# Kernel optimization log

Hardware: AMD Instinct MI355X
Metric: run time of the kernel (lower is better)

Reference implementation:

```python
import jax, jax.numpy as jnp
import numpy as np

FRACTION = 0.33  # from attn_type='query_selector_0.33'


def setup_inputs() -> dict:
    key = jax.random.key(0)
    k1, k2, k3, k4 = jax.random.split(key, 4)
    B, L, DIM_VAL, DIM_ATTN = 8, 4096, 64, 64
    scale = 1.0 / np.sqrt(DIM_VAL).astype(np.float32)
    x = jax.random.normal(k1, (B, L, DIM_VAL), dtype=jnp.float32)
    Wq = jax.random.normal(k2, (DIM_VAL, DIM_ATTN), dtype=jnp.float32) * scale
    Wk = jax.random.normal(k3, (DIM_VAL, DIM_ATTN), dtype=jnp.float32) * scale
    Wv = jax.random.normal(k4, (DIM_VAL, DIM_VAL), dtype=jnp.float32) * scale
    return {"x": x, "Wq": Wq, "Wk": Wk, "Wv": Wv}


def reference(x, Wq, Wk, Wv):
    # Projections (bias-free Linears)
    Q = jnp.einsum('bld,de->ble', x, Wq)  # [B, L, Da]
    K = jnp.einsum('bld,de->ble', x, Wk)  # [B, L, Da]
    V = jnp.einsum('bld,de->ble', x, Wv)  # [B, L, Dv]

    B, L_Q, Da = Q.shape
    l_Q = int((1.0 - FRACTION) * L_Q)  # static: shapes known at trace time

    # keys.topk(l_Q, dim=1).values -> per-channel top-l_Q along seq; mean over them
    K_top = jax.lax.top_k(jnp.swapaxes(K, 1, 2), l_Q)[0]  # [B, Da, l_Q]
    K_reduce = K_top.mean(axis=-1)                         # [B, Da]

    # score each query against the reduced key; pick top-l_Q queries
    sqk = jnp.einsum('bd,bld->bl', K_reduce, Q)            # [B, L_Q]
    indices = jax.lax.top_k(sqk, l_Q)[1]                   # [B, l_Q] int32

    # gather sampled queries
    Q_sample = jnp.take_along_axis(Q, indices[:, :, None], axis=1)  # [B, l_Q, Da]

    # dense attention for the sampled queries only
    scores = jnp.einsum('bqd,bkd->bqk', Q_sample, K) / jnp.sqrt(jnp.asarray(Da, Q.dtype))
    attn = jax.nn.softmax(scores, axis=-1)                 # [B, l_Q, L]
    out_sel = jnp.einsum('bqk,bkv->bqv', attn, V)          # [B, l_Q, Dv]

    # mean-filled result, scatter attention outputs to selected rows
    mean_values = V.mean(axis=-2)                          # [B, Dv]
    result = jnp.broadcast_to(mean_values[:, None, :], (B, L_Q, V.shape[-1]))
    result = result.at[jnp.arange(B)[:, None], indices].set(out_sel)
    return result
```

## Files before the change

kernel.cpp:

```cpp
#include <hip/hip_runtime.h>
#include <hip/hip_bf16.h>
#include <math.h>

#define BATCH 8
#define SEQ   4096
#define DIM   64
#define LQ    2744
#define QPB   128
#define NQB   22
#define QPAD  2816
#define KS    8
#define L2E   1.4426950408889634f
#define QSC   0.1803368801111204f

typedef _Float16 half8 __attribute__((ext_vector_type(8)));
typedef short    bs8   __attribute__((ext_vector_type(8)));
typedef float    fx16  __attribute__((ext_vector_type(16)));
typedef unsigned short ushort_t;

union UH { uint4 u4; half8 h; };
union UB { unsigned u[4]; uint4 u4; bs8 s; };

__device__ __forceinline__ unsigned pack_bf16(float a, float b) {
    unsigned ua = __float_as_uint(a), ub = __float_as_uint(b);
    ua += 0x7FFFu + ((ua >> 16) & 1u);
    ub += 0x7FFFu + ((ub >> 16) & 1u);
    return (ua >> 16) | (ub & 0xFFFF0000u);
}

__device__ __forceinline__ unsigned f2sort(float f) {
    unsigned u = __float_as_uint(f);
    return (u & 0x80000000u) ? ~u : (u | 0x80000000u);
}
__device__ __forceinline__ float sort2f(unsigned u) {
    return __uint_as_float((u & 0x80000000u) ? (u & 0x7FFFFFFFu) : ~u);
}

template <int NT>
__device__ void radix_select_4096(const unsigned* u, int k, unsigned* hist,
                                  unsigned* scan, unsigned* res) {
    const int t = threadIdx.x;
    if (t == 0) { res[0] = 0u; res[1] = (unsigned)k; }
    for (int pass = 3; pass >= 0; --pass) {
        const int shift = pass * 8;
        if (t < 256) hist[t] = 0u;
        __syncthreads();
        const unsigned pref  = res[0];
        const unsigned kk    = res[1];
        const unsigned hmask = (pass == 3) ? 0u : (0xFFFFFFFFu << (shift + 8));
        for (int i = t; i < 4096; i += NT) {
            unsigned ui = u[i];
            if ((ui & hmask) == pref) atomicAdd(&hist[(ui >> shift) & 255u], 1u);
        }
        __syncthreads();
        unsigned h = 0u, s = 0u;
        if (t < 256) { h = hist[t]; s = h; scan[t] = s; }
        __syncthreads();
#pragma unroll
        for (int ofs = 1; ofs < 256; ofs <<= 1) {
            unsigned add = (t < 256 && t + ofs < 256) ? scan[t + ofs] : 0u;
            __syncthreads();
            if (t < 256) { s += add; scan[t] = s; }
            __syncthreads();
        }
        if (t < 256 && s >= kk && (s - h) < kk) {
            res[0] = pref | ((unsigned)t << shift);
            res[1] = kk - (s - h);
        }
        __syncthreads();
    }
}

__global__ __launch_bounds__(256) void proj_kernel(
    const float* __restrict__ x,  const float* __restrict__ Wq,
    const float* __restrict__ Wk, const float* __restrict__ Wv,
    float* __restrict__ Q, float* __restrict__ Kt,
    _Float16* __restrict__ Qh, _Float16* __restrict__ Kh,
    ushort_t* __restrict__ Vt, float* __restrict__ pmean) {
    const int rt = blockIdx.x, b = blockIdx.y, t = threadIdx.x;
    __shared__ float4 xs4[64 * 17];
    __shared__ float  red[4][64];
    {
        const float4* xg = (const float4*)(x + ((size_t)b * SEQ + rt * 64) * DIM);
        for (int i = 0; i < 4; ++i) {
            int s = t + 256 * i;
            xs4[(s >> 4) * 17 + (s & 15)] = xg[s];
        }
    }
    __syncthreads();
    const int ch = t & 63, rg = t >> 6;
    float accq[16], acck[16], accv[16];
#pragma unroll
    for (int i = 0; i < 16; ++i) { accq[i] = 0.f; acck[i] = 0.f; accv[i] = 0.f; }
    for (int dc = 0; dc < 4; ++dc) {
        float wq[16], wk[16], wv[16];
#pragma unroll
        for (int dd = 0; dd < 16; ++dd) {
            int d = dc * 16 + dd;
            wq[dd] = Wq[d * 64 + ch]; wk[dd] = Wk[d * 64 + ch]; wv[dd] = Wv[d * 64 + ch];
        }
        for (int r = 0; r < 16; ++r) {
            const int row = rg * 16 + r;
            const float4* xr = &xs4[row * 17 + dc * 4];
            float xv[16];
            float4 a0 = xr[0], a1 = xr[1], a2 = xr[2], a3 = xr[3];
            xv[0]=a0.x; xv[1]=a0.y; xv[2]=a0.z; xv[3]=a0.w;
            xv[4]=a1.x; xv[5]=a1.y; xv[6]=a1.z; xv[7]=a1.w;
            xv[8]=a2.x; xv[9]=a2.y; xv[10]=a2.z; xv[11]=a2.w;
            xv[12]=a3.x; xv[13]=a3.y; xv[14]=a3.z; xv[15]=a3.w;
#pragma unroll
            for (int dd = 0; dd < 16; ++dd) {
                accq[r] = fmaf(xv[dd], wq[dd], accq[r]);
                acck[r] = fmaf(xv[dd], wk[dd], acck[r]);
                accv[r] = fmaf(xv[dd], wv[dd], accv[r]);
            }
        }
    }
    const int rowbase = rt * 64 + rg * 16;
    float sv = 0.f;
#pragma unroll
    for (int r = 0; r < 16; ++r) {
        size_t o = ((size_t)b * SEQ + rowbase + r) * DIM + ch;
        Q[o]  = accq[r];
        Qh[o] = (_Float16)(accq[r] * QSC);
        Kh[o] = (_Float16)acck[r];
        sv += accv[r];
    }
    float4* ktp = (float4*)(Kt + ((size_t)b * 64 + ch) * SEQ + rowbase);
    ktp[0] = make_float4(acck[0], acck[1], acck[2], acck[3]);
    ktp[1] = make_float4(acck[4], acck[5], acck[6], acck[7]);
    ktp[2] = make_float4(acck[8], acck[9], acck[10], acck[11]);
    ktp[3] = make_float4(acck[12], acck[13], acck[14], acck[15]);
    {
        unsigned pk[8];
#pragma unroll
        for (int i = 0; i < 8; ++i) {
            __hip_bfloat162 h2 = __float22bfloat162_rn(make_float2(accv[2*i], accv[2*i+1]));
            union { __hip_bfloat162 h; unsigned u; } cv; cv.h = h2;
            pk[i] = cv.u;
        }
        uint4* vp = (uint4*)(Vt + ((size_t)(b * 64 + ch)) * SEQ + rowbase);
        vp[0] = make_uint4(pk[0], pk[1], pk[4], pk[5]);
        vp[1] = make_uint4(pk[2], pk[3], pk[6], pk[7]);
    }
    red[rg][ch] = sv;
    __syncthreads();
    if (rg == 0)
        pmean[((size_t)b * 64 + ch) * 64 + rt] =
            red[0][ch] + red[1][ch] + red[2][ch] + red[3][ch];
}

__global__ __launch_bounds__(1024) void kmean_kernel(const float* __restrict__ Kt,
                                                     const float* __restrict__ pmean,
                                                     float* __restrict__ Kred,
                                                     float* __restrict__ meanfin) {
    __shared__ unsigned u[4096];
    __shared__ unsigned hist[256];
    __shared__ unsigned scan[256];
    __shared__ unsigned res[2];
    __shared__ float rsum[16];
    const int bc = blockIdx.x, t = threadIdx.x;
    if (t < 64) {
        float v = pmean[(size_t)bc * 64 + t];
        for (int m = 1; m < 64; m <<= 1) v += __shfl_xor(v, m, 64);
        if (t == 0) meanfin[bc] = v * (1.0f / (float)SEQ);
    }
    const float4* c4 = (const float4*)(Kt + (size_t)bc * SEQ);
    if (t < 1024) {
        float4 v = c4[t];
        u[t*4+0] = f2sort(v.x); u[t*4+1] = f2sort(v.y);
        u[t*4+2] = f2sort(v.z); u[t*4+3] = f2sort(v.w);
    }
    __syncthreads();
    radix_select_4096<1024>(u, LQ, hist, scan, res);
    const unsigned Tu = res[0];
    const int krem = (int)res[1];
    float loc = 0.f;
    for (int i = t; i < 4096; i += 1024)
        if (u[i] > Tu) loc += sort2f(u[i]);
    for (int msk = 1; msk < 64; msk <<= 1) loc += __shfl_xor(loc, msk, 64);
    if ((t & 63) == 0) rsum[t >> 6] = loc;
    __syncthreads();
    if (t == 0) {
        float s = (float)krem * sort2f(Tu);
        for (int i = 0; i < 16; ++i) s += rsum[i];
        Kred[bc] = s / (float)LQ;
    }
}

__global__ __launch_bounds__(1024) void select_kernel(const float* __restrict__ Q,
                                                      const float* __restrict__ Kred,
                                                      int* __restrict__ sel,
                                                      int* __restrict__ inv) {
    __shared__ unsigned u[4096];
    __shared__ unsigned hist[256];
    __shared__ unsigned scan[256];
    __shared__ unsigned res[2];
    __shared__ float kr[64];
    __shared__ int eq_idx[256];
    __shared__ int cnts[2];
    const int b = blockIdx.x, t = threadIdx.x;
    if (t < 64) kr[t] = Kred[b * 64 + t];
    if (t < 2) cnts[t] = 0;
    int* invb = inv + (size_t)b * SEQ;
    __syncthreads();
    for (int row = t; row < 4096; row += 1024) {
        const float4* q = (const float4*)(Q + ((size_t)b * SEQ + row) * DIM);
        float s = 0.f;
#pragma unroll
        for (int i = 0; i < 16; ++i) {
            float4 v = q[i];
            s = fmaf(v.x, kr[i*4+0], s); s = fmaf(v.y, kr[i*4+1], s);
            s = fmaf(v.z, kr[i*4+2], s); s = fmaf(v.w, kr[i*4+3], s);
        }
        u[row] = f2sort(s);
        invb[row] = -1;
    }
    __syncthreads();
    radix_select_4096<1024>(u, LQ, hist, scan, res);
    const unsigned Tu = res[0];
    const int krem = (int)res[1];
    int* selb = sel + b * QPAD;
    for (int i = t; i < 4096; i += 1024) {
        unsigned ui = u[i];
        if (ui > Tu) {
            int p = atomicAdd(&cnts[0], 1);
            selb[p] = i;
            invb[i] = p;
        } else if (ui == Tu) {
            int p = atomicAdd(&cnts[1], 1);
            if (p < 256) eq_idx[p] = i;
        }
    }
    __syncthreads();
    if (t == 0) {
        int ng = cnts[0];
        int ne = cnts[1] < 256 ? cnts[1] : 256;
        for (int i = 1; i < ne; ++i) {
            int v = eq_idx[i], j = i - 1;
            while (j >= 0 && eq_idx[j] > v) { eq_idx[j+1] = eq_idx[j]; --j; }
            eq_idx[j+1] = v;
        }
        for (int j = 0; j < krem; ++j) {
            selb[ng + j] = eq_idx[j];
            invb[eq_idx[j]] = ng + j;
        }
    }
    __syncthreads();
    if (t < QPAD - LQ) selb[LQ + t] = selb[LQ - 1];
}

__global__ __launch_bounds__(256, 3) void attn_kernel(
    const ushort_t* __restrict__ Qh, const ushort_t* __restrict__ Kh,
    const ushort_t* __restrict__ Vt, const int* __restrict__ sel,
    float* __restrict__ pl, float* __restrict__ pout) {
    const int qt = blockIdx.x, ks = blockIdx.y, b = blockIdx.z;
    const int t = threadIdx.x, w = t >> 6, lane = t & 63;
    const int col = lane & 31, h = lane >> 5;

    __shared__ ushort_t Ktile[2][32 * 64];
    __shared__ ushort_t Vtile[2][32 * 64];

    half8 qf[4];
    {
        const int q = qt * QPB + w * 32 + col;
        const int row = sel[b * QPAD + q];
        const uint4* qg = (const uint4*)(Qh + ((size_t)b * SEQ + row) * DIM);
#pragma unroll
        for (int m = 0; m < 4; ++m) { UH u; u.u4 = qg[2 * m + h]; qf[m] = u.h; }
    }

    int koff[4], voff[4];
#pragma unroll
    for (int m = 0; m < 4; ++m)
        koff[m] = col * 64 + 8 * ((2 * m + h) ^ (col & 7));
#pragma unroll
    for (int i = 0; i < 4; ++i)
        voff[i] = col * 64 + 8 * ((i * 2 + h) ^ (col & 7));

    fx16 O0, O1;
#pragma unroll
    for (int r = 0; r < 16; ++r) { O0[r] = 0.f; O1[r] = 0.f; }
    float l = 0.f;

    const int srow = t >> 3, sgr = t & 7;
    const int lg = sgr ^ (srow & 7);
    const int vD = lg >> 2, vc = (lg >> 1) & 1, vh = lg & 1;
    const size_t kgbase = ((size_t)b * SEQ + ks * 512 + srow) * DIM + 8 * lg;
    const size_t vgbase = ((size_t)(b * DIM + srow + 32 * vD)) * SEQ
                          + ks * 512 + vc * 16 + vh * 8;

    uint4 kreg = *(const uint4*)(Kh + kgbase);
    uint4 vreg = *(const uint4*)(Vt + vgbase);

    for (int tile = 0; tile < 16; ++tile) {
        const int buf = tile & 1;
        *(uint4*)&Ktile[buf][srow * 64 + sgr * 8] = kreg;
        *(uint4*)&Vtile[buf][srow * 64 + sgr * 8] = vreg;
        __syncthreads();
        if (tile < 15) {
            kreg = *(const uint4*)(Kh + kgbase + (size_t)(tile + 1) * 32 * DIM);
            vreg = *(const uint4*)(Vt + vgbase + (size_t)(tile + 1) * 32);
        }
        fx16 S;
#pragma unroll
        for (int r = 0; r < 16; ++r) S[r] = 0.f;
#pragma unroll
        for (int m = 0; m < 4; ++m) {
            UH kf;
            kf.u4 = *(const uint4*)&Ktile[buf][koff[m]];
            S = __builtin_amdgcn_mfma_f32_32x32x16_f16(kf.h, qf[m], S, 0, 0, 0);
        }
        float p[16];
#pragma unroll
        for (int r = 0; r < 16; ++r) p[r] = __builtin_amdgcn_exp2f(S[r]);
#pragma unroll
        for (int r = 0; r < 16; ++r) l += p[r];
        UB A0, A1;
#pragma unroll
        for (int v = 0; v < 4; ++v) {
            A0.u[v] = pack_bf16(p[2 * v],     p[2 * v + 1]);
            A1.u[v] = pack_bf16(p[8 + 2 * v], p[8 + 2 * v + 1]);
        }
#pragma unroll
        for (int D = 0; D < 2; ++D) {
            fx16& O = D ? O1 : O0;
#pragma unroll
            for (int c = 0; c < 2; ++c) {
                UB vf;
                vf.u4 = *(const uint4*)&Vtile[buf][voff[D * 2 + c]];
                O = __builtin_amdgcn_mfma_f32_32x32x16_bf16(c ? A1.s : A0.s, vf.s, O, 0, 0, 0);
            }
        }
    }

    l += __shfl_xor(l, 32);

    const int qg0 = qt * QPB + w * 32;
    const size_t base = (size_t)b * QPAD + qg0;
#pragma unroll
    for (int D = 0; D < 2; ++D) {
        const fx16& O = D ? O1 : O0;
#pragma unroll
        for (int r = 0; r < 16; ++r) {
            const int q = (r & 3) + 8 * (r >> 2) + 4 * h;
            atomicAdd(&pout[(base + q) * DIM + D * 32 + col], O[r]);
        }
    }
    if (h == 0) atomicAdd(&pl[base + col], l);
}

__global__ __launch_bounds__(256) void comb_kernel(
    const float* __restrict__ pl, const float* __restrict__ pout,
    const int* __restrict__ inv, const float* __restrict__ meanfin,
    float* __restrict__ out) {
    const int idx = blockIdx.x * 256 + threadIdx.x;
    const int b = idx >> 16;
    const int rc = idx & 65535;
    const int row = rc >> 4, c = rc & 15;
    const int p = inv[b * SEQ + row];
    float4 o;
    if (p >= 0) {
        const size_t s0 = (size_t)b * QPAD + p;
        const float invl = 1.0f / pl[s0];
        float4 a = ((const float4*)(pout + s0 * DIM))[c];
        o = make_float4(a.x * invl, a.y * invl, a.z * invl, a.w * invl);
    } else {
        o = make_float4(meanfin[b * 64 + c * 4 + 0], meanfin[b * 64 + c * 4 + 1],
                        meanfin[b * 64 + c * 4 + 2], meanfin[b * 64 + c * 4 + 3]);
    }
    ((float4*)out)[idx] = o;
}

extern "C" void kernel_launch(void* const* d_in, const int* in_sizes, int n_in,
                              void* d_out, int out_size, void* d_ws, size_t ws_size,
                              hipStream_t stream) {
    const float* x  = (const float*)d_in[0];
    const float* Wq = (const float*)d_in[1];
    const float* Wk = (const float*)d_in[2];
    const float* Wv = (const float*)d_in[3];
    float* out = (float*)d_out;
    char* wsb  = (char*)d_ws;

    float*    Q       = (float*)(wsb);
    _Float16* Qh      = (_Float16*)(wsb + 8388608);
    _Float16* Kh      = (_Float16*)(wsb + 12582912);
    ushort_t* Vt      = (ushort_t*)(wsb + 16777216);
    float*    pmean   = (float*)(wsb + 20971520);
    float*    meanfin = (float*)(wsb + 21102592);
    float*    Kred    = (float*)(wsb + 21104640);
    int*      sel     = (int*)(wsb + 21106688);
    int*      inv     = (int*)(wsb + 21196800);
    float*    Kt      = (float*)(wsb + 21327872);
    float*    pout    = (float*)(wsb + 21327872);
    float*    pl      = (float*)(wsb + 21327872 + 5767168);

    proj_kernel  <<<dim3(64, 8),          256,  0, stream>>>(x, Wq, Wk, Wv, Q, Kt,
                                                             Qh, Kh, Vt, pmean);
    kmean_kernel <<<512,                  1024, 0, stream>>>(Kt, pmean, Kred, meanfin);
    select_kernel<<<8,                    1024, 0, stream>>>(Q, Kred, sel, inv);
    hipMemsetAsync(pout, 0, 5767168 + 90112, stream);
    attn_kernel  <<<dim3(NQB, KS, BATCH), 256,  0, stream>>>((const ushort_t*)Qh,
                                                             (const ushort_t*)Kh,
                                                             Vt, sel, pl, pout);
    comb_kernel  <<<2048,                 256,  0, stream>>>(pl, pout, inv, meanfin, out);
}
```

Baseline: 220.6 us.

## Fold output zeroing into kmean, switch P·V to fp16, shrink select blocks

Removes the separate memset: each kmean block zeroes its own slice of the aliased pout/pl buffer after copying its Kt slice into shared memory. V and the softmax probabilities now use fp16 with the hardware round-toward-zero packed convert instead of software bf16 rounding, so the P·V MFMA runs in f16. The kmean and select kernels drop from 1024 to 256 threads per block. That may help kmean occupancy, but it quadruples per-thread work in the 8-block select kernel, which is latency-bound. fp16 also has less exponent range than bf16 for V values and exp2 outputs.

```diff
diff --git a/kernel.cpp b/kernel.cpp
--- a/kernel.cpp
+++ b/kernel.cpp
@@ -1,5 +1,4 @@
 #include <hip/hip_runtime.h>
-#include <hip/hip_bf16.h>
 #include <math.h>
 
 #define BATCH 8
@@ -10,22 +9,19 @@
 #define NQB   22
 #define QPAD  2816
 #define KS    8
-#define L2E   1.4426950408889634f
 #define QSC   0.1803368801111204f
+#define PZN   1464320
 
 typedef _Float16 half8 __attribute__((ext_vector_type(8)));
-typedef short    bs8   __attribute__((ext_vector_type(8)));
+typedef __fp16   fp16x2 __attribute__((ext_vector_type(2)));
 typedef float    fx16  __attribute__((ext_vector_type(16)));
 typedef unsigned short ushort_t;
 
-union UH { uint4 u4; half8 h; };
-union UB { unsigned u[4]; uint4 u4; bs8 s; };
-
-__device__ __forceinline__ unsigned pack_bf16(float a, float b) {
-    unsigned ua = __float_as_uint(a), ub = __float_as_uint(b);
-    ua += 0x7FFFu + ((ua >> 16) & 1u);
-    ub += 0x7FFFu + ((ub >> 16) & 1u);
-    return (ua >> 16) | (ub & 0xFFFF0000u);
+union UHF { unsigned u[4]; uint4 u4; half8 h; };
+
+__device__ __forceinline__ unsigned pack_f16(float a, float b) {
+    fp16x2 r = __builtin_amdgcn_cvt_pkrtz(a, b);
+    union { fp16x2 h; unsigned u; } cv; cv.h = r; return cv.u;
 }
 
 __device__ __forceinline__ unsigned f2sort(float f) {
@@ -100,8 +96,7 @@
             wq[dd] = Wq[d * 64 + ch]; wk[dd] = Wk[d * 64 + ch]; wv[dd] = Wv[d * 64 + ch];
         }
         for (int r = 0; r < 16; ++r) {
-            const int row = rg * 16 + r;
-            const float4* xr = &xs4[row * 17 + dc * 4];
+            const float4* xr = &xs4[(rg * 16 + r) * 17 + dc * 4];
             float xv[16];
             float4 a0 = xr[0], a1 = xr[1], a2 = xr[2], a3 = xr[3];
             xv[0]=a0.x; xv[1]=a0.y; xv[2]=a0.z; xv[3]=a0.w;
@@ -134,11 +129,7 @@
     {
         unsigned pk[8];
 #pragma unroll
-        for (int i = 0; i < 8; ++i) {
-            __hip_bfloat162 h2 = __float22bfloat162_rn(make_float2(accv[2*i], accv[2*i+1]));
-            union { __hip_bfloat162 h; unsigned u; } cv; cv.h = h2;
-            pk[i] = cv.u;
-        }
+        for (int i = 0; i < 8; ++i) pk[i] = pack_f16(accv[2*i], accv[2*i+1]);
         uint4* vp = (uint4*)(Vt + ((size_t)(b * 64 + ch)) * SEQ + rowbase);
         vp[0] = make_uint4(pk[0], pk[1], pk[4], pk[5]);
         vp[1] = make_uint4(pk[2], pk[3], pk[6], pk[7]);
@@ -150,15 +141,16 @@
             red[0][ch] + red[1][ch] + red[2][ch] + red[3][ch];
 }
 
-__global__ __launch_bounds__(1024) void kmean_kernel(const float* __restrict__ Kt,
-                                                     const float* __restrict__ pmean,
-                                                     float* __restrict__ Kred,
-                                                     float* __restrict__ meanfin) {
+__global__ __launch_bounds__(256) void kmean_kernel(const float* __restrict__ Kt,
+                                                    const float* __restrict__ pmean,
+                                                    float* __restrict__ Kred,
+                                                    float* __restrict__ meanfin,
+                                                    float* __restrict__ poutz) {
     __shared__ unsigned u[4096];
     __shared__ unsigned hist[256];
     __shared__ unsigned scan[256];
     __shared__ unsigned res[2];
-    __shared__ float rsum[16];
+    __shared__ float rsum[4];
     const int bc = blockIdx.x, t = threadIdx.x;
     if (t < 64) {
         float v = pmean[(size_t)bc * 64 + t];
@@ -166,32 +158,41 @@
         if (t == 0) meanfin[bc] = v * (1.0f / (float)SEQ);
     }
     const float4* c4 = (const float4*)(Kt + (size_t)bc * SEQ);
-    if (t < 1024) {
-        float4 v = c4[t];
-        u[t*4+0] = f2sort(v.x); u[t*4+1] = f2sort(v.y);
-        u[t*4+2] = f2sort(v.z); u[t*4+3] = f2sort(v.w);
-    }
-    __syncthreads();
-    radix_select_4096<1024>(u, LQ, hist, scan, res);
+    for (int i = t; i < 1024; i += 256) {
+        float4 v = c4[i];
+        u[i*4+0] = f2sort(v.x); u[i*4+1] = f2sort(v.y);
+        u[i*4+2] = f2sort(v.z); u[i*4+3] = f2sort(v.w);
+    }
+    __syncthreads();
+    {
+        const int zbase = bc * 4096;
+        if (zbase < PZN) {
+            const int zend = (zbase + 4096 < PZN) ? zbase + 4096 : PZN;
+            float4* z4 = (float4*)(poutz + zbase);
+            const int n4 = (zend - zbase) >> 2;
+            const float4 zz = make_float4(0.f, 0.f, 0.f, 0.f);
+            for (int i = t; i < n4; i += 256) z4[i] = zz;
+        }
+    }
+    radix_select_4096<256>(u, LQ, hist, scan, res);
     const unsigned Tu = res[0];
     const int krem = (int)res[1];
     float loc = 0.f;
-    for (int i = t; i < 4096; i += 1024)
+    for (int i = t; i < 4096; i += 256)
         if (u[i] > Tu) loc += sort2f(u[i]);
     for (int msk = 1; msk < 64; msk <<= 1) loc += __shfl_xor(loc, msk, 64);
     if ((t & 63) == 0) rsum[t >> 6] = loc;
     __syncthreads();
     if (t == 0) {
-        float s = (float)krem * sort2f(Tu);
-        for (int i = 0; i < 16; ++i) s += rsum[i];
+        float s = rsum[0] + rsum[1] + rsum[2] + rsum[3] + (float)krem * sort2f(Tu);
         Kred[bc] = s / (float)LQ;
     }
 }
 
-__global__ __launch_bounds__(1024) void select_kernel(const float* __restrict__ Q,
-                                                      const float* __restrict__ Kred,
-                                                      int* __restrict__ sel,
-                                                      int* __restrict__ inv) {
+__global__ __launch_bounds__(256) void select_kernel(const float* __restrict__ Q,
+                                                     const float* __restrict__ Kred,
+                                                     int* __restrict__ sel,
+                                                     int* __restrict__ inv) {
     __shared__ unsigned u[4096];
     __shared__ unsigned hist[256];
     __shared__ unsigned scan[256];
@@ -204,7 +205,7 @@
     if (t < 2) cnts[t] = 0;
     int* invb = inv + (size_t)b * SEQ;
     __syncthreads();
-    for (int row = t; row < 4096; row += 1024) {
+    for (int row = t; row < 4096; row += 256) {
         const float4* q = (const float4*)(Q + ((size_t)b * SEQ + row) * DIM);
         float s = 0.f;
 #pragma unroll
@@ -217,11 +218,11 @@
         invb[row] = -1;
     }
     __syncthreads();
-    radix_select_4096<1024>(u, LQ, hist, scan, res);
+    radix_select_4096<256>(u, LQ, hist, scan, res);
     const unsigned Tu = res[0];
     const int krem = (int)res[1];
     int* selb = sel + b * QPAD;
-    for (int i = t; i < 4096; i += 1024) {
+    for (int i = t; i < 4096; i += 256) {
         unsigned ui = u[i];
         if (ui > Tu) {
             int p = atomicAdd(&cnts[0], 1);
@@ -267,7 +268,7 @@
         const int row = sel[b * QPAD + q];
         const uint4* qg = (const uint4*)(Qh + ((size_t)b * SEQ + row) * DIM);
 #pragma unroll
-        for (int m = 0; m < 4; ++m) { UH u; u.u4 = qg[2 * m + h]; qf[m] = u.h; }
+        for (int m = 0; m < 4; ++m) { UHF u; u.u4 = qg[2 * m + h]; qf[m] = u.h; }
     }
 
     int koff[4], voff[4];
@@ -307,7 +308,7 @@
         for (int r = 0; r < 16; ++r) S[r] = 0.f;
 #pragma unroll
         for (int m = 0; m < 4; ++m) {
-            UH kf;
+            UHF kf;
             kf.u4 = *(const uint4*)&Ktile[buf][koff[m]];
             S = __builtin_amdgcn_mfma_f32_32x32x16_f16(kf.h, qf[m], S, 0, 0, 0);
         }
@@ -316,20 +317,20 @@
         for (int r = 0; r < 16; ++r) p[r] = __builtin_amdgcn_exp2f(S[r]);
 #pragma unroll
         for (int r = 0; r < 16; ++r) l += p[r];
-        UB A0, A1;
+        UHF A0, A1;
 #pragma unroll
         for (int v = 0; v < 4; ++v) {
-            A0.u[v] = pack_bf16(p[2 * v],     p[2 * v + 1]);
-            A1.u[v] = pack_bf16(p[8 + 2 * v], p[8 + 2 * v + 1]);
+            A0.u[v] = pack_f16(p[2 * v],     p[2 * v + 1]);
+            A1.u[v] = pack_f16(p[8 + 2 * v], p[8 + 2 * v + 1]);
         }
 #pragma unroll
         for (int D = 0; D < 2; ++D) {
             fx16& O = D ? O1 : O0;
 #pragma unroll
             for (int c = 0; c < 2; ++c) {
-                UB vf;
+                UHF vf;
                 vf.u4 = *(const uint4*)&Vtile[buf][voff[D * 2 + c]];
-                O = __builtin_amdgcn_mfma_f32_32x32x16_bf16(c ? A1.s : A0.s, vf.s, O, 0, 0, 0);
+                O = __builtin_amdgcn_mfma_f32_32x32x16_f16(c ? A1.h : A0.h, vf.h, O, 0, 0, 0);
             }
         }
     }
@@ -395,13 +396,13 @@
     float*    pout    = (float*)(wsb + 21327872);
     float*    pl      = (float*)(wsb + 21327872 + 5767168);
 
-    proj_kernel  <<<dim3(64, 8),          256,  0, stream>>>(x, Wq, Wk, Wv, Q, Kt,
-                                                             Qh, Kh, Vt, pmean);
-    kmean_kernel <<<512,                  1024, 0, stream>>>(Kt, pmean, Kred, meanfin);
-    select_kernel<<<8,                    1024, 0, stream>>>(Q, Kred, sel, inv);
-    hipMemsetAsync(pout, 0, 5767168 + 90112, stream);
-    attn_kernel  <<<dim3(NQB, KS, BATCH), 256,  0, stream>>>((const ushort_t*)Qh,
-                                                             (const ushort_t*)Kh,
-                                                             Vt, sel, pl, pout);
-    comb_kernel  <<<2048,                 256,  0, stream>>>(pl, pout, inv, meanfin, out);
-}
+    proj_kernel  <<<dim3(64, 8),          256, 0, stream>>>(x, Wq, Wk, Wv, Q, Kt,
+                                                            Qh, Kh, Vt, pmean);
+    kmean_kernel <<<512,                  256, 0, stream>>>(Kt, pmean, Kred,
+                                                            meanfin, pout);
+    select_kernel<<<8,                    256, 0, stream>>>(Q, Kred, sel, inv);
+    attn_kernel  <<<dim3(NQB, KS, BATCH), 256, 0, stream>>>((const ushort_t*)Qh,
+                                                            (const ushort_t*)Kh,
+                                                            Vt, sel, pl, pout);
+    comb_kernel  <<<2048,                 256, 0, stream>>>(pl, pout, inv, meanfin, out);
+}
```

New measurement: 209.0 us. 1.06x faster.
